# Performance work log

Hardware: AMD Instinct MI355X
Metric: run time of the kernel (lower is better)

The kernel has to match this reference:

```python
import jax, jax.numpy as jnp
import numpy as np

I3 = jnp.eye(3, dtype=jnp.float32)
G_VEC = jnp.array([0.0, 0.0, -9.80665], dtype=jnp.float32)
# Q diag: [cov_omega x3, cov_acc x3, cov_b_omega x3, cov_b_acc x3, cov_Rot_c_i x3, cov_t_c_i x3]
Q_DIAG = jnp.array([1e-3] * 3 + [1e-2] * 3 + [6e-9] * 3 + [2e-4] * 3 + [1e-9] * 3 + [1e-9] * 3, dtype=jnp.float32)
N_NORM_ROT = 100
N_NORM_ROT_CI = 1000


def skew(v):
    z = jnp.zeros_like(v[0])
    return jnp.stack([jnp.stack([z, -v[2], v[1]]),
                      jnp.stack([v[2], z, -v[0]]),
                      jnp.stack([-v[1], v[0], z])])


def so3exp(phi):
    a2 = jnp.sum(phi * phi)
    small = a2 < 1e-12
    a = jnp.sqrt(jnp.where(small, 1.0, a2))
    axis = phi / a
    c, s = jnp.cos(a), jnp.sin(a)
    big = c * I3 + (1.0 - c) * jnp.outer(axis, axis) + s * skew(axis)
    return jnp.where(small, I3 + skew(phi), big)


def sen3exp(xi):
    # SE_2(3) exponential: xi[:3]=rotation, xi[3:9]=(v, p) parts
    phi = xi[:3]
    a2 = jnp.sum(phi * phi)
    small = a2 < 1e-12
    a = jnp.sqrt(jnp.where(small, 1.0, a2))
    axis = phi / a
    c, s = jnp.cos(a), jnp.sin(a)
    sk = skew(axis)
    R = jnp.where(small, I3 + skew(phi),
                  c * I3 + (1.0 - c) * jnp.outer(axis, axis) + s * sk)
    J = jnp.where(small, I3 + 0.5 * skew(phi),
                  (s / a) * I3 + (1.0 - s / a) * jnp.outer(axis, axis) + ((1.0 - c) / a) * sk)
    x = J @ xi[3:].reshape(2, 3).T  # (3,2): columns are dv, dp
    return R, x


def normalize_rot(R):
    # Polar-factor re-orthonormalization (equivalent to the SVD-based
    # normalize_rot for near-rotation matrices), via Newton-Schulz iteration
    # which is smooth and jit/vjp friendly.
    def body(X, _):
        return 1.5 * X - 0.5 * (X @ X.T @ X), None
    X, _ = jax.lax.scan(body, R, None, length=8)
    return X


def from_rpy(roll, pitch, yaw):
    cr, sr = jnp.cos(roll), jnp.sin(roll)
    cp, sp = jnp.cos(pitch), jnp.sin(pitch)
    cy, sy = jnp.cos(yaw), jnp.sin(yaw)
    one = jnp.ones_like(cr)
    zero = jnp.zeros_like(cr)
    Rx = jnp.stack([jnp.stack([one, zero, zero]), jnp.stack([zero, cr, -sr]), jnp.stack([zero, sr, cr])])
    Ry = jnp.stack([jnp.stack([cp, zero, sp]), jnp.stack([zero, one, zero]), jnp.stack([-sp, zero, cp])])
    Rz = jnp.stack([jnp.stack([cy, -sy, zero]), jnp.stack([sy, cy, zero]), jnp.stack([zero, zero, one])])
    return Rz @ Ry @ Rx


def init_covariance():
    P = jnp.zeros((21, 21), dtype=jnp.float32)
    P = P.at[:2, :2].set(1e-3 * jnp.eye(2))     # cov_Rot0 (no yaw error)
    P = P.at[3:5, 3:5].set(0.1 * jnp.eye(2))    # cov_v0
    P = P.at[9:12, 9:12].set(6e-3 * I3)         # cov_b_omega0
    P = P.at[12:15, 12:15].set(4e-3 * I3)       # cov_b_acc0
    P = P.at[15:18, 15:18].set(1e-6 * I3)       # cov_Rot_c_i0
    P = P.at[18:21, 18:21].set(5e-3 * I3)       # cov_t_c_i0
    return P


def propagate_cov(P, Rot, v, p, dt):
    F = jnp.zeros((21, 21), dtype=P.dtype)
    F = F.at[3:6, :3].set(skew(G_VEC))
    F = F.at[6:9, 3:6].set(I3)
    F = F.at[:3, 9:12].set(-Rot)
    F = F.at[3:6, 9:12].set(-skew(v) @ Rot)
    F = F.at[3:6, 12:15].set(-Rot)
    F = F.at[6:9, 9:12].set(-skew(p) @ Rot)
    G = jnp.zeros((21, 18), dtype=P.dtype)
    G = G.at[:3, :3].set(Rot)
    G = G.at[3:6, 3:6].set(Rot)
    G = G.at[9:12, 6:9].set(I3)
    G = G.at[12:15, 9:12].set(I3)
    G = G.at[15:18, 12:15].set(I3)
    G = G.at[18:21, 15:18].set(I3)
    F = F * dt
    G = G * dt
    F2 = F @ F
    Phi = jnp.eye(21, dtype=P.dtype) + F + 0.5 * F2 + (F2 @ F) / 6.0  # 3rd-order expm
    return Phi @ (P + (G * Q_DIAG[None, :]) @ G.T) @ Phi.T


def _step(carry, xs):
    Rot, v, p, b_om, b_ac, Rci, tci, P = carry
    u_i, dt_i, mcov_i, i = xs
    # ---- propagate ----
    acc = Rot @ (u_i[3:6] - b_ac) + G_VEC
    v_n = v + acc * dt_i
    p_n = p + v * dt_i + 0.5 * acc * dt_i * dt_i
    Rot_n = Rot @ so3exp((u_i[:3] - b_om) * dt_i)
    P_n = propagate_cov(P, Rot, v, p, dt_i)
    # ---- update: zero lateral/vertical body-velocity pseudo-measurement ----
    omega = u_i[:3] - b_om
    Rot_body = Rot_n @ Rci
    v_imu = Rot_n.T @ v_n
    v_body = Rci.T @ v_imu + skew(tci) @ omega
    H = jnp.zeros((2, 21), dtype=P.dtype)
    H = H.at[:, 3:6].set(Rot_body.T[1:])
    H = H.at[:, 15:18].set((Rci.T @ skew(v_imu))[1:])
    H = H.at[:, 9:12].set(skew(tci)[1:])
    H = H.at[:, 18:21].set(-skew(omega)[1:])
    r = -v_body[1:]
    Rm = jnp.diag(mcov_i)
    S = H @ P_n @ H.T + Rm                    # (2,2)
    K = jnp.linalg.solve(S, H @ P_n).T        # K = P H^T S^-1 (P, S symmetric)
    dx = K @ r                                 # (21,)
    dR, dxi = sen3exp(dx[:9])
    Rot_u = dR @ Rot_n
    v_u = dR @ v_n + dxi[:, 0]
    p_u = dR @ p_n + dxi[:, 1]
    b_om_u = b_om + dx[9:12]
    b_ac_u = b_ac + dx[12:15]
    Rci_u = so3exp(dx[15:18]) @ Rci
    tci_u = tci + dx[18:21]
    IKH = jnp.eye(21, dtype=P.dtype) - K @ H
    P_u = IKH @ P_n @ IKH.T + K @ Rm @ K.T    # Joseph form
    P_u = 0.5 * (P_u + P_u.T)
    Rot_u = jnp.where(i % N_NORM_ROT == 0, normalize_rot(Rot_u), Rot_u)
    Rci_u = jnp.where(i % N_NORM_ROT_CI == 0, normalize_rot(Rci_u), Rci_u)
    carry = (Rot_u, v_u, p_u, b_om_u, b_ac_u, Rci_u, tci_u, P_u)
    return carry, (Rot_u, v_u, p_u, b_om_u, b_ac_u, Rci_u, tci_u)


def _forward(t, u, measurements_covs, v_mes, p_mes, ang0, N):
    dt = t[1:N] - t[:N - 1]
    Rot0 = from_rpy(ang0[0], ang0[1], ang0[2])
    z3 = jnp.zeros(3, dtype=u.dtype)
    carry0 = (Rot0, v_mes[0], z3, z3, z3, I3, z3, init_covariance())
    xs = (u[1:N], dt, measurements_covs[1:N], jnp.arange(1, N))
    _, ys = jax.lax.scan(_step, carry0, xs)
    Rot = jnp.concatenate([Rot0[None], ys[0]], axis=0)
    v = jnp.concatenate([v_mes[0][None], ys[1]], axis=0)
    p = jnp.concatenate([z3[None], ys[2]], axis=0)
    b_omega = jnp.concatenate([z3[None], ys[3]], axis=0)
    b_acc = jnp.concatenate([z3[None], ys[4]], axis=0)
    Rot_c_i = jnp.concatenate([I3[None], ys[5]], axis=0)
    t_c_i = jnp.concatenate([z3[None], ys[6]], axis=0)
    return (Rot, v, p, b_omega, b_acc, Rot_c_i, t_c_i)


def setup_inputs() -> dict:
    key = jax.random.key(0)
    N = 20000  # 200 s at 100 Hz IMU
    k0, k1, k2, k3, k4, k5 = jax.random.split(key, 6)
    t = jnp.arange(N, dtype=jnp.float32) * 0.01
    gyro = 0.01 * jax.random.normal(k0, (N, 3), dtype=jnp.float32)
    acc = jnp.array([0.0, 0.0, 9.80665], jnp.float32) + 0.1 * jax.random.normal(k1, (N, 3), dtype=jnp.float32)
    u = jnp.concatenate([gyro, acc], axis=1)
    measurements_covs = 0.1 + jax.random.uniform(k2, (N, 2), dtype=jnp.float32)
    v_mes = jax.random.normal(k3, (N, 3), dtype=jnp.float32)
    p_mes = jax.random.normal(k4, (N, 3), dtype=jnp.float32)
    ang0 = 0.01 * jax.random.normal(k5, (3,), dtype=jnp.float32)
    return dict(t=t, u=u, measurements_covs=measurements_covs, v_mes=v_mes, p_mes=p_mes, ang0=ang0, N=N)


def reference(t, u, measurements_covs, v_mes, p_mes, ang0, N):
    return _forward(t, u, measurements_covs, v_mes, p_mes, ang0, N)
```

## Files before the change

### kernel.cpp

```cpp
#include <hip/hip_runtime.h>

#define GRAV 9.80665f
#define WAVE_SYNC() do { \
    asm volatile("s_waitcnt lgkmcnt(0)" ::: "memory"); \
    __builtin_amdgcn_sched_barrier(0); \
  } while(0)

__device__ __forceinline__ float sel3(int r, float a0, float a1, float a2){
  float x = (r==1)? a1 : a0;
  return (r>=2)? a2 : x;
}
__device__ __forceinline__ float RL(float v, int k){
  return __int_as_float(__builtin_amdgcn_readlane(__float_as_int(v), k));
}
__device__ __forceinline__ float pick9(int k, const float* X){
  float s=X[0];
  s=(k==1)?X[1]:s; s=(k==2)?X[2]:s; s=(k==3)?X[3]:s; s=(k==4)?X[4]:s;
  s=(k==5)?X[5]:s; s=(k==6)?X[6]:s; s=(k==7)?X[7]:s; s=(k==8)?X[8]:s;
  return s;
}

__device__ __forceinline__ void mm33(float* __restrict__ O, const float* A, const float* B){
#pragma unroll
  for(int r=0;r<3;++r){
#pragma unroll
    for(int c=0;c<3;++c){
      O[r*3+c] = A[r*3+0]*B[0*3+c] + A[r*3+1]*B[1*3+c] + A[r*3+2]*B[2*3+c];
    }
  }
}

__device__ __forceinline__ void rot_from_t2(float t_, float p0, float p1, float p2, float* R){
  float c_, k1_, k2_;
  if (t_ < 1e-4f){
    c_  = 1.f - t_*(0.5f - t_*((1.f/24.f) - t_*(1.f/720.f)));
    k2_ = 1.f - t_*((1.f/6.f) - t_*((1.f/120.f) - t_*(1.f/5040.f)));
    k1_ = 0.5f - t_*((1.f/24.f) - t_*(1.f/720.f));
  } else {
    float a = sqrtf(t_);
    c_ = __cosf(a);
    float s = __sinf(a);
    k2_ = s/a;
    k1_ = (1.f - c_)/t_;
  }
  R[0]=c_+k1_*p0*p0;      R[1]=k1_*p0*p1-k2_*p2;  R[2]=k1_*p0*p2+k2_*p1;
  R[3]=k1_*p0*p1+k2_*p2;  R[4]=c_+k1_*p1*p1;      R[5]=k1_*p1*p2-k2_*p0;
  R[6]=k1_*p0*p2-k2_*p1;  R[7]=k1_*p1*p2+k2_*p0;  R[8]=c_+k1_*p2*p2;
}

__device__ __forceinline__ void normalize_rot9(float* X){
#pragma unroll 1
  for(int it=0; it<8; ++it){
    float Y[9], Z[9];
#pragma unroll
    for(int r=0;r<3;++r)
#pragma unroll
      for(int c=0;c<3;++c)
        Y[r*3+c] = X[r*3+0]*X[c*3+0] + X[r*3+1]*X[c*3+1] + X[r*3+2]*X[c*3+2];
#pragma unroll
    for(int r=0;r<3;++r)
#pragma unroll
      for(int c=0;c<3;++c)
        Z[r*3+c] = Y[r*3+0]*X[0*3+c] + Y[r*3+1]*X[1*3+c] + Y[r*3+2]*X[2*3+c];
#pragma unroll
    for(int e=0;e<9;++e) X[e] = 1.5f*X[e] - 0.5f*Z[e];
  }
}

__device__ __forceinline__ float pick_state(int l,
    const float* Rt, const float* vv, const float* pp,
    const float* bw, const float* ba, const float* Rc, const float* tc){
  float s = Rt[0];
  s=(l==1)?Rt[1]:s;  s=(l==2)?Rt[2]:s;  s=(l==3)?Rt[3]:s;  s=(l==4)?Rt[4]:s;
  s=(l==5)?Rt[5]:s;  s=(l==6)?Rt[6]:s;  s=(l==7)?Rt[7]:s;  s=(l==8)?Rt[8]:s;
  s=(l==9)?vv[0]:s;  s=(l==10)?vv[1]:s; s=(l==11)?vv[2]:s;
  s=(l==12)?pp[0]:s; s=(l==13)?pp[1]:s; s=(l==14)?pp[2]:s;
  s=(l==15)?bw[0]:s; s=(l==16)?bw[1]:s; s=(l==17)?bw[2]:s;
  s=(l==18)?ba[0]:s; s=(l==19)?ba[1]:s; s=(l==20)?ba[2]:s;
  s=(l==21)?Rc[0]:s; s=(l==22)?Rc[1]:s; s=(l==23)?Rc[2]:s;
  s=(l==24)?Rc[3]:s; s=(l==25)?Rc[4]:s; s=(l==26)?Rc[5]:s;
  s=(l==27)?Rc[6]:s; s=(l==28)?Rc[7]:s; s=(l==29)?Rc[8]:s;
  s=(l==30)?tc[0]:s; s=(l==31)?tc[1]:s; s=(l==32)?tc[2]:s;
  return s;
}

__global__ __launch_bounds__(64,1)
void iekf_scan_kernel(const float* __restrict__ t,
                      const float* __restrict__ u,
                      const float* __restrict__ mcov,
                      const float* __restrict__ v_mes,
                      const float* __restrict__ ang0,
                      float* __restrict__ out, int N)
{
  const int l = threadIdx.x;
  __shared__ float  Pm[441];
  __shared__ float  Eb[441];
  __shared__ float  PnS[441];
  __shared__ float2 HPs2[21];
  __shared__ __align__(16) float stS[36];

  for (int e=l; e<441; e+=64){
    int r=e/21, c=e-(e/21)*21;
    float vI=0.f;
    if (r==c){
      if (r<2) vI=0.001f;
      else if (r==3||r==4) vI=0.1f;
      else if (r>=9&&r<12) vI=0.006f;
      else if (r>=12&&r<15) vI=0.004f;
      else if (r>=15&&r<18) vI=1e-6f;
      else if (r>=18) vI=0.005f;
    }
    Pm[e]=vI;
  }

  int ostr=0; float* op = out;
  {
    int obase=0, ooff=0;
    if (l<9)       {obase=0;    ostr=9; ooff=l;}
    else if (l<12) {obase=9*N;  ostr=3; ooff=l-9;}
    else if (l<15) {obase=12*N; ostr=3; ooff=l-12;}
    else if (l<18) {obase=15*N; ostr=3; ooff=l-15;}
    else if (l<21) {obase=18*N; ostr=3; ooff=l-18;}
    else if (l<30) {obase=21*N; ostr=9; ooff=l-21;}
    else           {obase=30*N; ostr=3; ooff=l-30;}
    op = out + obase + ooff;
  }

  const int g21 = l/21;
  const int c21 = l - g21*21;
  const int cw  = 9 + 4*g21;
  int l1 = l+21; if (l1>=63) l1-=63;
  int l2 = l+42; if (l2>=63) l2-=63;
  static const int cols[12] = {3,4,5, 9,10,11, 15,16,17, 18,19,20};

  {
    float Rt0[9], vv0[3], pp0[3], bwa[3], baa[3], Rc0[9], tca[3];
    float rl = ang0[0], pt = ang0[1], yw = ang0[2];
    float cr=cosf(rl), sr=sinf(rl), cp=cosf(pt), sp=sinf(pt), cy=cosf(yw), sy=sinf(yw);
    Rt0[0]=cy*cp; Rt0[1]=cy*sp*sr - sy*cr; Rt0[2]=cy*sp*cr + sy*sr;
    Rt0[3]=sy*cp; Rt0[4]=sy*sp*sr + cy*cr; Rt0[5]=sy*sp*cr - cy*sr;
    Rt0[6]=-sp;   Rt0[7]=cp*sr;            Rt0[8]=cp*cr;
    vv0[0]=v_mes[0]; vv0[1]=v_mes[1]; vv0[2]=v_mes[2];
#pragma unroll
    for(int k=0;k<3;++k){ pp0[k]=0.f; bwa[k]=0.f; baa[k]=0.f; tca[k]=0.f; }
    Rc0[0]=1.f;Rc0[1]=0.f;Rc0[2]=0.f;Rc0[3]=0.f;Rc0[4]=1.f;Rc0[5]=0.f;Rc0[6]=0.f;Rc0[7]=0.f;Rc0[8]=1.f;
    float sv = pick_state(l, Rt0, vv0, pp0, bwa, baa, Rc0, tca);
    if (l<33){ op[0] = sv; stS[l] = sv; }
    if (l>=33 && l<36) stS[l] = 0.f;
  }
  WAVE_SYNC();

  float tA = t[0], tB = t[1];
  float cu[6];
#pragma unroll
  for(int k=0;k<6;++k) cu[k]=u[6+k];
  float cm0=mcov[2], cm1=mcov[3];

  int nx100=100, nx1000=1000;

#pragma unroll 1
  for (int i=1; i<N; ++i){
    float dt = tB - tA;
    float u0=cu[0], u1=cu[1], u2=cu[2], u3=cu[3], u4=cu[4], u5=cu[5];
    float crm0=cm0, crm1=cm1;
    if (i+1 < N){
      tA = tB; tB = t[i+1];
#pragma unroll
      for(int k=0;k<6;++k) cu[k]=u[(i+1)*6+k];
      cm0 = mcov[(i+1)*2]; cm1 = mcov[(i+1)*2+1];
    }

    const float4* st4 = (const float4*)stS;
    float4 q0=st4[0], q1=st4[1], q2=st4[2], q3=st4[3], q4=st4[4], q5=st4[5], q6=st4[6], q7=st4[7], q8=st4[8];
    float Rt[9] = {q0.x,q0.y,q0.z,q0.w,q1.x,q1.y,q1.z,q1.w,q2.x};
    float vv0s=q2.y, vv1s=q2.z, vv2s=q2.w;
    float pp0s=q3.x, pp1s=q3.y, pp2s=q3.z;
    float bw0=q3.w, bw1=q4.x, bw2=q4.y;
    float ba0=q4.z, ba1=q4.w, ba2=q5.x;
    float Rc[9] = {q5.y,q5.z,q5.w,q6.x,q6.y,q6.z,q6.w,q7.x,q7.y};
    float tc0=q7.z, tc1=q7.w, tc2=q8.x;

    float dt2=dt*dt, gdt=GRAV*dt, hdt=0.5f*dt, hdt2=0.5f*dt*dt;
    float hgdt2 = 0.5f*gdt*dt;
    float g6d   = gdt*dt2*(1.0f/6.0f);

    float w0=u0-bw0, w1=u1-bw1, w2=u2-bw2;
    float aa0=u3-ba0, aa1=u4-ba1, aa2=u5-ba2;
    float acc0 = Rt[0]*aa0+Rt[1]*aa1+Rt[2]*aa2;
    float acc1 = Rt[3]*aa0+Rt[4]*aa1+Rt[5]*aa2;
    float acc2 = Rt[6]*aa0+Rt[7]*aa1+Rt[8]*aa2 - GRAV;
    float vn0=vv0s+acc0*dt, vn1=vv1s+acc1*dt, vn2=vv2s+acc2*dt;
    float pn0=pp0s+vv0s*dt+acc0*hdt2;
    float pn1=pp1s+vv1s*dt+acc1*hdt2;
    float pn2=pp2s+vv2s*dt+acc2*hdt2;
    float ph0=w0*dt, ph1=w1*dt, ph2=w2*dt;
    float dRs[9]; rot_from_t2(ph0*ph0+ph1*ph1+ph2*ph2, ph0,ph1,ph2, dRs);
    float Rn[9]; mm33(Rn, Rt, dRs);

    float RtG[3], RtA[3], RtB[3];
#pragma unroll
    for(int k=0;k<3;++k){
      float r0=Rt[k], r3=Rt[3+k], r6=Rt[6+k];
      RtG[k] = sel3(g21, r0, r3, r6);
      RtA[k] = sel3(g21, r3, r6, r0);
      RtB[k] = sel3(g21, r6, r0, r3);
    }
    float vAs = sel3(g21, vv2s, vv0s, vv1s), vBs = sel3(g21, vv1s, vv2s, vv0s);
    float pAs = sel3(g21, pp2s, pp0s, pp1s), pBs = sel3(g21, pp1s, pp2s, pp0s);
    float Bs0,Bs1,Bs2, Cs0,Cs1,Cs2, Ds0,Ds1,Ds2;
    {
      float bs[3], cs[3], ds[3];
#pragma unroll
      for(int k=0;k<3;++k){
        bs[k] = -dt*RtG[k];
        float craw = dt*(vAs*RtA[k] - vBs*RtB[k]);
        float selC = sel3(g21, -RtA[k], RtB[k], 0.f);
        cs[k] = craw + hgdt2*selC;
        float draw = dt*(pAs*RtA[k] - pBs*RtB[k]);
        ds[k] = draw + hdt*craw + g6d*selC;
      }
      Bs0=bs[0];Bs1=bs[1];Bs2=bs[2];
      Cs0=cs[0];Cs1=cs[1];Cs2=cs[2];
      Ds0=ds[0];Ds1=ds[1];Ds2=ds[2];
    }

    float q0d=0.001f*dt2, q1d=0.01f*dt2;
    float q69=6e-9f*dt2, q24=2e-4f*dt2, q19=1e-9f*dt2;

    if (l<63){
      int c = c21;
      bool cl3 = (c<3);
      bool c36 = (c>=3 && c<6);
      int csel = c36 ? (c-3) : (cl3 ? c : 0);
      float Rtc0 = sel3(csel, Rt[0], Rt[3], Rt[6]);
      float Rtc1 = sel3(csel, Rt[1], Rt[4], Rt[7]);
      float Rtc2 = sel3(csel, Rt[2], Rt[5], Rt[8]);
      float dot0 = Rt[0]*Rtc0 + Rt[1]*Rtc1 + Rt[2]*Rtc2;
      float dot1 = Rt[3]*Rtc0 + Rt[4]*Rtc1 + Rt[5]*Rtc2;
      float dotg = RtG[0]*Rtc0 + RtG[1]*Rtc1 + RtG[2]*Rtc2;
      float d0  = cl3 ? q0d*dot0 : 0.f;
      float d1  = cl3 ? q0d*dot1 : 0.f;
      float dg  = cl3 ? q0d*dotg : 0.f;
      float dg3 = c36 ? q1d*dotg : 0.f;

      float m0  = Pm[c]            + d0;
      float m1  = Pm[21+c]         + d1;
      float mr  = Pm[g21*21+c]     + dg;
      float m3r = Pm[(3+g21)*21+c] + dg3;
      float m6r = Pm[(6+g21)*21+c];
      float m9  = Pm[9*21+c]  + ((c==9) ? q69 : 0.f);
      float m10 = Pm[10*21+c] + ((c==10)? q69 : 0.f);
      float m11 = Pm[11*21+c] + ((c==11)? q69 : 0.f);
      float m12 = Pm[12*21+c] + ((c==12)? q24 : 0.f);
      float m13 = Pm[13*21+c] + ((c==13)? q24 : 0.f);
      float m14 = Pm[14*21+c] + ((c==14)? q24 : 0.f);

      float Ar = (g21==0)? gdt*m1 : (g21==1)? -gdt*m0 : 0.f;
      float bterm = Bs0*m12+Bs1*m13+Bs2*m14;
      float e0 = mr + Bs0*m9+Bs1*m10+Bs2*m11;
      float e1 = m3r + Ar + Cs0*m9+Cs1*m10+Cs2*m11 + bterm;
      float e2 = m6r + hdt*Ar + dt*m3r + Ds0*m9+Ds1*m10+Ds2*m11 + hdt*bterm;
      Eb[g21*21+c]=e0; Eb[(3+g21)*21+c]=e1; Eb[(6+g21)*21+c]=e2;
#pragma unroll
      for (int jj=0;jj<4;++jj){
        int row = cw+jj;
        float qd = (row<12)? q69 : (row<15)? q24 : q19;
        Eb[row*21+c] = Pm[row*21+c] + ((row==c)? qd : 0.f);
      }
    }

    float H0[12], H1[12];
    float vi0, vi1, vi2, rr0, rr1;
    {
      float Rb1 = Rn[0]*Rc[1]+Rn[1]*Rc[4]+Rn[2]*Rc[7];
      float Rb4 = Rn[3]*Rc[1]+Rn[4]*Rc[4]+Rn[5]*Rc[7];
      float Rb7 = Rn[6]*Rc[1]+Rn[7]*Rc[4]+Rn[8]*Rc[7];
      float Rb2 = Rn[0]*Rc[2]+Rn[1]*Rc[5]+Rn[2]*Rc[8];
      float Rb5 = Rn[3]*Rc[2]+Rn[4]*Rc[5]+Rn[5]*Rc[8];
      float Rb8 = Rn[6]*Rc[2]+Rn[7]*Rc[5]+Rn[8]*Rc[8];
      vi0 = Rn[0]*vn0+Rn[3]*vn1+Rn[6]*vn2;
      vi1 = Rn[1]*vn0+Rn[4]*vn1+Rn[7]*vn2;
      vi2 = Rn[2]*vn0+Rn[5]*vn1+Rn[8]*vn2;
      float vb1 = Rc[1]*vi0+Rc[4]*vi1+Rc[7]*vi2 + (tc2*w0 - tc0*w2);
      float vb2 = Rc[2]*vi0+Rc[5]*vi1+Rc[8]*vi2 + (tc0*w1 - tc1*w0);
      rr0 = -vb1; rr1 = -vb2;
      H0[0]=Rb1; H0[1]=Rb4; H0[2]=Rb7;
      H1[0]=Rb2; H1[1]=Rb5; H1[2]=Rb8;
      H0[3]=tc2;  H0[4]=0.f;  H0[5]=-tc0;
      H1[3]=-tc1; H1[4]=tc0;  H1[5]=0.f;
      H0[6]=Rc[4]*vi2 - Rc[7]*vi1;  H0[7]=Rc[7]*vi0 - Rc[1]*vi2;  H0[8]=Rc[1]*vi1 - Rc[4]*vi0;
      H1[6]=Rc[5]*vi2 - Rc[8]*vi1;  H1[7]=Rc[8]*vi0 - Rc[2]*vi2;  H1[8]=Rc[2]*vi1 - Rc[5]*vi0;
      H0[9]=-w2; H0[10]=0.f; H0[11]=w0;
      H1[9]=w1;  H1[10]=-w0; H1[11]=0.f;
    }
    WAVE_SYNC();

    float pnv[7];
#pragma unroll
    for(int k=0;k<7;++k) pnv[k]=0.f;
    float p0=0.f, p1=0.f;
    if (l<63){
      int r = c21;
      const float* Er = Eb + r*21;
      float e0a=Er[0], e1a=Er[1];
      float eg=Er[g21], e3g=Er[3+g21], e6g=Er[6+g21];
      float e9=Er[9],e10=Er[10],e11=Er[11],e12=Er[12],e13=Er[13],e14=Er[14];
      float Ag = (g21==0)? gdt*e1a : (g21==1)? -gdt*e0a : 0.f;
      float bterm = Bs0*e12+Bs1*e13+Bs2*e14;
      pnv[0] = eg + Bs0*e9+Bs1*e10+Bs2*e11;
      pnv[1] = e3g + Ag + Cs0*e9+Cs1*e10+Cs2*e11 + bterm;
      pnv[2] = e6g + hdt*Ag + dt*e3g + Ds0*e9+Ds1*e10+Ds2*e11 + hdt*bterm;
      pnv[3] = Er[cw]; pnv[4] = Er[cw+1]; pnv[5] = Er[cw+2]; pnv[6] = Er[cw+3];

      PnS[r*21 + g21]   = pnv[0];
      PnS[r*21 + 3+g21] = pnv[1];
      PnS[r*21 + 6+g21] = pnv[2];
      PnS[r*21 + cw]    = pnv[3];
      PnS[r*21 + cw+1]  = pnv[4];
      PnS[r*21 + cw+2]  = pnv[5];
      PnS[r*21 + cw+3]  = pnv[6];

      float c1a = sel3(g21, H0[0], H0[1], H0[2]);
      float c3a = sel3(g21, H0[3], 0.f,   H0[8]);
      float c4a = sel3(g21, H0[4], 0.f,   H0[9]);
      float c5a = sel3(g21, H0[5], H0[6], H0[10]);
      float c6a = sel3(g21, 0.f,   H0[7], H0[11]);
      float c1b = sel3(g21, H1[0], H1[1], H1[2]);
      float c3b = sel3(g21, H1[3], 0.f,   H1[8]);
      float c4b = sel3(g21, H1[4], 0.f,   H1[9]);
      float c5b = sel3(g21, H1[5], H1[6], H1[10]);
      float c6b = sel3(g21, 0.f,   H1[7], H1[11]);
      p0 = c1a*pnv[1] + c3a*pnv[3] + c4a*pnv[4] + c5a*pnv[5] + c6a*pnv[6];
      p1 = c1b*pnv[1] + c3b*pnv[3] + c4b*pnv[4] + c5b*pnv[5] + c6b*pnv[6];
    }
    float hpr0 = p0 + __shfl(p0, l1) + __shfl(p0, l2);
    float hpr1 = p1 + __shfl(p1, l1) + __shfl(p1, l2);
    if (l<21) HPs2[l] = make_float2(hpr0, hpr1);

    float hph00=0.f, hph01=0.f, hph10=0.f, hph11=0.f;
#pragma unroll
    for(int k=0;k<12;++k){
      float hp0 = RL(hpr0, cols[k]);
      float hp1 = RL(hpr1, cols[k]);
      hph00 += hp0*H0[k]; hph01 += hp0*H1[k];
      hph10 += hp1*H0[k]; hph11 += hp1*H1[k];
    }
    float s00 = hph00 + crm0, s01 = hph01, s10 = hph10, s11 = hph11 + crm1;
    float idet = 1.0f/(s00*s11 - s01*s10);
    float i00 =  s11*idet, i01 = -s01*idet, i10 = -s10*idet, i11 = s00*idet;
    float K0 = i00*hpr0 + i01*hpr1;
    float K1 = i10*hpr0 + i11*hpr1;
    float s01q = 0.5f*(s01 + s10);
    float dxval = K0*rr0 + K1*rr1;

    float dx0 = RL(dxval,0), dx1 = RL(dxval,1), dx2 = RL(dxval,2);
    float dx3 = RL(dxval,3), dx4 = RL(dxval,4), dx5 = RL(dxval,5);
    float dx6 = RL(dxval,6), dx7 = RL(dxval,7), dx8 = RL(dxval,8);
    float dx15 = RL(dxval,15), dx16 = RL(dxval,16), dx17 = RL(dxval,17);
    int src = (l>=30 && l<33)? (l-12) : ((l>=15 && l<21)? (l-6) : 0);
    float dxadd = __shfl(dxval, src);

    float t2x = dx0*dx0+dx1*dx1+dx2*dx2;
    float cX,k1X,k2X,j1X;
    if (t2x < 1e-4f){
      cX  = 1.f - t2x*(0.5f - t2x*((1.f/24.f) - t2x*(1.f/720.f)));
      k2X = 1.f - t2x*((1.f/6.f) - t2x*((1.f/120.f) - t2x*(1.f/5040.f)));
      k1X = 0.5f - t2x*((1.f/24.f) - t2x*(1.f/720.f));
      j1X = (1.f/6.f) - t2x*((1.f/120.f) - t2x*(1.f/5040.f));
    } else {
      float a = sqrtf(t2x);
      cX = __cosf(a);
      float s = __sinf(a);
      k2X = s/a; k1X = (1.f-cX)/t2x; j1X = (1.f-k2X)/t2x;
    }
    float dR[9];
    dR[0]=cX+k1X*dx0*dx0;      dR[1]=k1X*dx0*dx1-k2X*dx2; dR[2]=k1X*dx0*dx2+k2X*dx1;
    dR[3]=k1X*dx0*dx1+k2X*dx2; dR[4]=cX+k1X*dx1*dx1;      dR[5]=k1X*dx1*dx2-k2X*dx0;
    dR[6]=k1X*dx0*dx2-k2X*dx1; dR[7]=k1X*dx1*dx2+k2X*dx0; dR[8]=cX+k1X*dx2*dx2;
    float Jm[9];
    Jm[0]=k2X+j1X*dx0*dx0;      Jm[1]=j1X*dx0*dx1-k1X*dx2; Jm[2]=j1X*dx0*dx2+k1X*dx1;
    Jm[3]=j1X*dx0*dx1+k1X*dx2;  Jm[4]=k2X+j1X*dx1*dx1;     Jm[5]=j1X*dx1*dx2-k1X*dx0;
    Jm[6]=j1X*dx0*dx2-k1X*dx1;  Jm[7]=j1X*dx1*dx2+k1X*dx0; Jm[8]=k2X+j1X*dx2*dx2;
    float Ec[9];
    rot_from_t2(dx15*dx15+dx16*dx16+dx17*dx17, dx15,dx16,dx17, Ec);

    WAVE_SYNC();

    if (l<63){
      int r = c21;
#pragma unroll
      for (int s=0;s<7;++s){
        int j = (s<3)? (g21 + 3*s) : (cw + (s-3));
        float pnT = PnS[j*21 + r];
        float2 hpj = HPs2[j];
        float kjx = i00*hpj.x + i01*hpj.y;
        float kjy = i10*hpj.x + i11*hpj.y;
        float base  = 0.5f*(pnv[s] + pnT);
        float cross = (K0*hpj.x + K1*hpj.y) + (kjx*hpr0 + kjy*hpr1);
        float quad  = (K0*kjx)*s00 + (K0*kjy + K1*kjx)*s01q + (K1*kjy)*s11;
        Pm[r*21+j] = base - cross + quad;
      }
    }

    float myval = 0.f;
    if (l<9){
      int ro=(l>=6)?2:((l>=3)?1:0); int co=l-3*ro;
      float d0=sel3(ro,dR[0],dR[3],dR[6]), d1=sel3(ro,dR[1],dR[4],dR[7]), d2=sel3(ro,dR[2],dR[5],dR[8]);
      float n0=sel3(co,Rn[0],Rn[1],Rn[2]), n1=sel3(co,Rn[3],Rn[4],Rn[5]), n2=sel3(co,Rn[6],Rn[7],Rn[8]);
      myval = d0*n0 + d1*n1 + d2*n2;
    } else if (l<15){
      int j=l-9; bool isv=(j<3); int ro = isv? j : (j-3);
      float x0 = isv? vn0:pn0, x1 = isv? vn1:pn1, x2 = isv? vn2:pn2;
      float y0 = isv? dx3:dx6, y1 = isv? dx4:dx7, y2 = isv? dx5:dx8;
      float d0=sel3(ro,dR[0],dR[3],dR[6]), d1=sel3(ro,dR[1],dR[4],dR[7]), d2=sel3(ro,dR[2],dR[5],dR[8]);
      float j0=sel3(ro,Jm[0],Jm[3],Jm[6]), j1m=sel3(ro,Jm[1],Jm[4],Jm[7]), j2m=sel3(ro,Jm[2],Jm[5],Jm[8]);
      myval = d0*x0 + d1*x1 + d2*x2 + j0*y0 + j1m*y1 + j2m*y2;
    } else if (l<21){
      float old = (l<18)? sel3(l-15,bw0,bw1,bw2) : sel3(l-18,ba0,ba1,ba2);
      myval = old + dxadd;
    } else if (l<30){
      int j=l-21; int ro=(j>=6)?2:((j>=3)?1:0); int co=j-3*ro;
      float e0=sel3(ro,Ec[0],Ec[3],Ec[6]), e1=sel3(ro,Ec[1],Ec[4],Ec[7]), e2=sel3(ro,Ec[2],Ec[5],Ec[8]);
      float r0=sel3(co,Rc[0],Rc[1],Rc[2]), r1=sel3(co,Rc[3],Rc[4],Rc[5]), r2=sel3(co,Rc[6],Rc[7],Rc[8]);
      myval = e0*r0 + e1*r1 + e2*r2;
    } else if (l<33){
      myval = sel3(l-30,tc0,tc1,tc2) + dxadd;
    }
    if (l<33) stS[l] = myval;

    bool n100 = (i==nx100), n1000 = (i==nx1000);
    if (n100) nx100 += 100;
    if (n1000) nx1000 += 1000;
    if (n100 || n1000){
      WAVE_SYNC();
      if (n100){
        float X[9];
#pragma unroll
        for (int k=0;k<9;++k) X[k]=stS[k];
        normalize_rot9(X);
        if (l<9){ myval = pick9(l,X); stS[l] = myval; }
      }
      if (n1000){
        float Y[9];
#pragma unroll
        for (int k=0;k<9;++k) Y[k]=stS[21+k];
        normalize_rot9(Y);
        if (l>=21 && l<30){ myval = pick9(l-21,Y); stS[l] = myval; }
      }
    }

    if (l<33) op[i*ostr] = myval;

    WAVE_SYNC();
  }
}

extern "C" void kernel_launch(void* const* d_in, const int* in_sizes, int n_in,
                              void* d_out, int out_size, void* d_ws, size_t ws_size,
                              hipStream_t stream) {
  (void)n_in; (void)out_size; (void)d_ws; (void)ws_size;
  const float* t     = (const float*)d_in[0];
  const float* u     = (const float*)d_in[1];
  const float* mcov  = (const float*)d_in[2];
  const float* v_mes = (const float*)d_in[3];
  const float* ang0  = (const float*)d_in[5];
  int N = in_sizes[0];
  iekf_scan_kernel<<<dim3(1), dim3(64), 0, stream>>>(t, u, mcov, v_mes, ang0, (float*)d_out, N);
}
```

Baseline: 44.76 ms.

## Keep filter state in registers and pad covariance rows for vector LDS loads

```diff
diff --git a/kernel.cpp b/kernel.cpp
--- a/kernel.cpp
+++ b/kernel.cpp
@@ -5,6 +5,8 @@
     asm volatile("s_waitcnt lgkmcnt(0)" ::: "memory"); \
     __builtin_amdgcn_sched_barrier(0); \
   } while(0)
+
+#define LDP 28
 
 __device__ __forceinline__ float sel3(int r, float a0, float a1, float a2){
   float x = (r==1)? a1 : a0;
@@ -93,14 +95,11 @@
                       float* __restrict__ out, int N)
 {
   const int l = threadIdx.x;
-  __shared__ float  Pm[441];
-  __shared__ float  Eb[441];
-  __shared__ float  PnS[441];
-  __shared__ float2 HPs2[21];
-  __shared__ __align__(16) float stS[36];
-
-  for (int e=l; e<441; e+=64){
-    int r=e/21, c=e-(e/21)*21;
+  __shared__ __align__(16) float Pm[21*LDP];
+  __shared__ __align__(16) float Eb[21*LDP];
+
+  for (int e=l; e<21*LDP; e+=64){
+    int r=e/LDP, c=e-(e/LDP)*LDP;
     float vI=0.f;
     if (r==c){
       if (r<2) vI=0.001f;
@@ -108,7 +107,7 @@
       else if (r>=9&&r<12) vI=0.006f;
       else if (r>=12&&r<15) vI=0.004f;
       else if (r>=15&&r<18) vI=1e-6f;
-      else if (r>=18) vI=0.005f;
+      else if (r>=18&&r<21) vI=0.005f;
     }
     Pm[e]=vI;
   }
@@ -133,6 +132,7 @@
   int l2 = l+42; if (l2>=63) l2-=63;
   static const int cols[12] = {3,4,5, 9,10,11, 15,16,17, 18,19,20};
 
+  float myval = 0.f;
   {
     float Rt0[9], vv0[3], pp0[3], bwa[3], baa[3], Rc0[9], tca[3];
     float rl = ang0[0], pt = ang0[1], yw = ang0[2];
@@ -145,8 +145,7 @@
     for(int k=0;k<3;++k){ pp0[k]=0.f; bwa[k]=0.f; baa[k]=0.f; tca[k]=0.f; }
     Rc0[0]=1.f;Rc0[1]=0.f;Rc0[2]=0.f;Rc0[3]=0.f;Rc0[4]=1.f;Rc0[5]=0.f;Rc0[6]=0.f;Rc0[7]=0.f;Rc0[8]=1.f;
     float sv = pick_state(l, Rt0, vv0, pp0, bwa, baa, Rc0, tca);
-    if (l<33){ op[0] = sv; stS[l] = sv; }
-    if (l>=33 && l<36) stS[l] = 0.f;
+    if (l<33){ op[0] = sv; myval = sv; }
   }
   WAVE_SYNC();
 
@@ -170,15 +169,17 @@
       cm0 = mcov[(i+1)*2]; cm1 = mcov[(i+1)*2+1];
     }
 
-    const float4* st4 = (const float4*)stS;
-    float4 q0=st4[0], q1=st4[1], q2=st4[2], q3=st4[3], q4=st4[4], q5=st4[5], q6=st4[6], q7=st4[7], q8=st4[8];
-    float Rt[9] = {q0.x,q0.y,q0.z,q0.w,q1.x,q1.y,q1.z,q1.w,q2.x};
-    float vv0s=q2.y, vv1s=q2.z, vv2s=q2.w;
-    float pp0s=q3.x, pp1s=q3.y, pp2s=q3.z;
-    float bw0=q3.w, bw1=q4.x, bw2=q4.y;
-    float ba0=q4.z, ba1=q4.w, ba2=q5.x;
-    float Rc[9] = {q5.y,q5.z,q5.w,q6.x,q6.y,q6.z,q6.w,q7.x,q7.y};
-    float tc0=q7.z, tc1=q7.w, tc2=q8.x;
+    float Rt[9];
+#pragma unroll
+    for(int k=0;k<9;++k) Rt[k] = RL(myval, k);
+    float vv0s=RL(myval,9),  vv1s=RL(myval,10), vv2s=RL(myval,11);
+    float pp0s=RL(myval,12), pp1s=RL(myval,13), pp2s=RL(myval,14);
+    float bw0=RL(myval,15),  bw1=RL(myval,16),  bw2=RL(myval,17);
+    float ba0=RL(myval,18),  ba1=RL(myval,19),  ba2=RL(myval,20);
+    float Rc[9];
+#pragma unroll
+    for(int k=0;k<9;++k) Rc[k] = RL(myval, 21+k);
+    float tc0=RL(myval,30), tc1=RL(myval,31), tc2=RL(myval,32);
 
     float dt2=dt*dt, gdt=GRAV*dt, hdt=0.5f*dt, hdt2=0.5f*dt*dt;
     float hgdt2 = 0.5f*gdt*dt;
@@ -229,6 +230,10 @@
 
     if (l<63){
       int c = c21;
+      const float4* Pr4 = (const float4*)(Pm + c*LDP);
+      float4 a0=Pr4[0], a1=Pr4[1], a2=Pr4[2], a3=Pr4[3], a4=Pr4[4];
+      float m20 = Pm[c*LDP + 20];
+
       bool cl3 = (c<3);
       bool c36 = (c>=3 && c<6);
       int csel = c36 ? (c-3) : (cl3 ? c : 0);
@@ -238,39 +243,42 @@
       float dot0 = Rt[0]*Rtc0 + Rt[1]*Rtc1 + Rt[2]*Rtc2;
       float dot1 = Rt[3]*Rtc0 + Rt[4]*Rtc1 + Rt[5]*Rtc2;
       float dotg = RtG[0]*Rtc0 + RtG[1]*Rtc1 + RtG[2]*Rtc2;
-      float d0  = cl3 ? q0d*dot0 : 0.f;
-      float d1  = cl3 ? q0d*dot1 : 0.f;
-      float dg  = cl3 ? q0d*dotg : 0.f;
-      float dg3 = c36 ? q1d*dotg : 0.f;
-
-      float m0  = Pm[c]            + d0;
-      float m1  = Pm[21+c]         + d1;
-      float mr  = Pm[g21*21+c]     + dg;
-      float m3r = Pm[(3+g21)*21+c] + dg3;
-      float m6r = Pm[(6+g21)*21+c];
-      float m9  = Pm[9*21+c]  + ((c==9) ? q69 : 0.f);
-      float m10 = Pm[10*21+c] + ((c==10)? q69 : 0.f);
-      float m11 = Pm[11*21+c] + ((c==11)? q69 : 0.f);
-      float m12 = Pm[12*21+c] + ((c==12)? q24 : 0.f);
-      float m13 = Pm[13*21+c] + ((c==13)? q24 : 0.f);
-      float m14 = Pm[14*21+c] + ((c==14)? q24 : 0.f);
+
+      float m0  = a0.x + (cl3 ? q0d*dot0 : 0.f);
+      float m1  = a0.y + (cl3 ? q0d*dot1 : 0.f);
+      float mr  = sel3(g21, a0.x, a0.y, a0.z) + (cl3 ? q0d*dotg : 0.f);
+      float m3r = sel3(g21, a0.w, a1.x, a1.y) + (c36 ? q1d*dotg : 0.f);
+      float m6r = sel3(g21, a1.z, a1.w, a2.x);
+      float m9  = a2.y + ((c==9) ? q69 : 0.f);
+      float m10 = a2.z + ((c==10)? q69 : 0.f);
+      float m11 = a2.w + ((c==11)? q69 : 0.f);
+      float m12 = a3.x + ((c==12)? q24 : 0.f);
+      float m13 = a3.y + ((c==13)? q24 : 0.f);
+      float m14 = a3.z + ((c==14)? q24 : 0.f);
 
       float Ar = (g21==0)? gdt*m1 : (g21==1)? -gdt*m0 : 0.f;
       float bterm = Bs0*m12+Bs1*m13+Bs2*m14;
       float e0 = mr + Bs0*m9+Bs1*m10+Bs2*m11;
       float e1 = m3r + Ar + Cs0*m9+Cs1*m10+Cs2*m11 + bterm;
       float e2 = m6r + hdt*Ar + dt*m3r + Ds0*m9+Ds1*m10+Ds2*m11 + hdt*bterm;
-      Eb[g21*21+c]=e0; Eb[(3+g21)*21+c]=e1; Eb[(6+g21)*21+c]=e2;
-#pragma unroll
-      for (int jj=0;jj<4;++jj){
-        int row = cw+jj;
-        float qd = (row<12)? q69 : (row<15)? q24 : q19;
-        Eb[row*21+c] = Pm[row*21+c] + ((row==c)? qd : 0.f);
-      }
+      Eb[g21*LDP+c]=e0; Eb[(3+g21)*LDP+c]=e1; Eb[(6+g21)*LDP+c]=e2;
+
+      float mc0 = sel3(g21, a2.y, a3.y, a4.y);
+      float mc1 = sel3(g21, a2.z, a3.z, a4.z);
+      float mc2 = sel3(g21, a2.w, a3.w, a4.w);
+      float mc3 = sel3(g21, a3.x, a4.x, m20);
+      float qd0 = sel3(g21, q69, q24, q19);
+      float qd1 = sel3(g21, q69, q24, q19);
+      float qd2 = sel3(g21, q69, q19, q19);
+      float qd3 = sel3(g21, q24, q19, q19);
+      Eb[(cw+0)*LDP+c] = mc0 + ((cw+0==c)? qd0 : 0.f);
+      Eb[(cw+1)*LDP+c] = mc1 + ((cw+1==c)? qd1 : 0.f);
+      Eb[(cw+2)*LDP+c] = mc2 + ((cw+2==c)? qd2 : 0.f);
+      Eb[(cw+3)*LDP+c] = mc3 + ((cw+3==c)? qd3 : 0.f);
     }
 
     float H0[12], H1[12];
-    float vi0, vi1, vi2, rr0, rr1;
+    float rr0, rr1;
     {
       float Rb1 = Rn[0]*Rc[1]+Rn[1]*Rc[4]+Rn[2]*Rc[7];
       float Rb4 = Rn[3]*Rc[1]+Rn[4]*Rc[4]+Rn[5]*Rc[7];
@@ -278,9 +286,9 @@
       float Rb2 = Rn[0]*Rc[2]+Rn[1]*Rc[5]+Rn[2]*Rc[8];
       float Rb5 = Rn[3]*Rc[2]+Rn[4]*Rc[5]+Rn[5]*Rc[8];
       float Rb8 = Rn[6]*Rc[2]+Rn[7]*Rc[5]+Rn[8]*Rc[8];
-      vi0 = Rn[0]*vn0+Rn[3]*vn1+Rn[6]*vn2;
-      vi1 = Rn[1]*vn0+Rn[4]*vn1+Rn[7]*vn2;
-      vi2 = Rn[2]*vn0+Rn[5]*vn1+Rn[8]*vn2;
+      float vi0 = Rn[0]*vn0+Rn[3]*vn1+Rn[6]*vn2;
+      float vi1 = Rn[1]*vn0+Rn[4]*vn1+Rn[7]*vn2;
+      float vi2 = Rn[2]*vn0+Rn[5]*vn1+Rn[8]*vn2;
       float vb1 = Rc[1]*vi0+Rc[4]*vi1+Rc[7]*vi2 + (tc2*w0 - tc0*w2);
       float vb2 = Rc[2]*vi0+Rc[5]*vi1+Rc[8]*vi2 + (tc0*w1 - tc1*w0);
       rr0 = -vb1; rr1 = -vb2;
@@ -301,24 +309,25 @@
     float p0=0.f, p1=0.f;
     if (l<63){
       int r = c21;
-      const float* Er = Eb + r*21;
-      float e0a=Er[0], e1a=Er[1];
-      float eg=Er[g21], e3g=Er[3+g21], e6g=Er[6+g21];
-      float e9=Er[9],e10=Er[10],e11=Er[11],e12=Er[12],e13=Er[13],e14=Er[14];
+      const float4* Er4 = (const float4*)(Eb + r*LDP);
+      float4 a0=Er4[0], a1=Er4[1], a2=Er4[2], a3=Er4[3], a4=Er4[4];
+      float e20 = Eb[r*LDP + 20];
+
+      float e0a=a0.x, e1a=a0.y;
+      float eg  = sel3(g21, a0.x, a0.y, a0.z);
+      float e3g = sel3(g21, a0.w, a1.x, a1.y);
+      float e6g = sel3(g21, a1.z, a1.w, a2.x);
+      float e9=a2.y, e10=a2.z, e11=a2.w, e12=a3.x, e13=a3.y, e14=a3.z;
+
       float Ag = (g21==0)? gdt*e1a : (g21==1)? -gdt*e0a : 0.f;
       float bterm = Bs0*e12+Bs1*e13+Bs2*e14;
       pnv[0] = eg + Bs0*e9+Bs1*e10+Bs2*e11;
       pnv[1] = e3g + Ag + Cs0*e9+Cs1*e10+Cs2*e11 + bterm;
       pnv[2] = e6g + hdt*Ag + dt*e3g + Ds0*e9+Ds1*e10+Ds2*e11 + hdt*bterm;
-      pnv[3] = Er[cw]; pnv[4] = Er[cw+1]; pnv[5] = Er[cw+2]; pnv[6] = Er[cw+3];
-
-      PnS[r*21 + g21]   = pnv[0];
-      PnS[r*21 + 3+g21] = pnv[1];
-      PnS[r*21 + 6+g21] = pnv[2];
-      PnS[r*21 + cw]    = pnv[3];
-      PnS[r*21 + cw+1]  = pnv[4];
-      PnS[r*21 + cw+2]  = pnv[5];
-      PnS[r*21 + cw+3]  = pnv[6];
+      pnv[3] = sel3(g21, a2.y, a3.y, a4.y);
+      pnv[4] = sel3(g21, a2.z, a3.z, a4.z);
+      pnv[5] = sel3(g21, a2.w, a3.w, a4.w);
+      pnv[6] = sel3(g21, a3.x, a4.x, e20);
 
       float c1a = sel3(g21, H0[0], H0[1], H0[2]);
       float c3a = sel3(g21, H0[3], 0.f,   H0[8]);
@@ -335,7 +344,14 @@
     }
     float hpr0 = p0 + __shfl(p0, l1) + __shfl(p0, l2);
     float hpr1 = p1 + __shfl(p1, l1) + __shfl(p1, l2);
-    if (l<21) HPs2[l] = make_float2(hpr0, hpr1);
+
+    float hpjx[7], hpjy[7];
+#pragma unroll
+    for (int s=0;s<7;++s){
+      int j = (s<3)? (g21 + 3*s) : (cw + (s-3));
+      hpjx[s] = __shfl(hpr0, j);
+      hpjy[s] = __shfl(hpr1, j);
+    }
 
     float hph00=0.f, hph01=0.f, hph10=0.f, hph11=0.f;
 #pragma unroll
@@ -359,6 +375,23 @@
     float dx15 = RL(dxval,15), dx16 = RL(dxval,16), dx17 = RL(dxval,17);
     int src = (l>=30 && l<33)? (l-12) : ((l>=15 && l<21)? (l-6) : 0);
     float dxadd = __shfl(dxval, src);
+
+    if (l<63){
+      int r = c21;
+#pragma unroll
+      for (int s=0;s<7;++s){
+        int j = (s<3)? (g21 + 3*s) : (cw + (s-3));
+        float kjx = i00*hpjx[s] + i01*hpjy[s];
+        float kjy = i10*hpjx[s] + i11*hpjy[s];
+        float cross = (K0*hpjx[s] + K1*hpjy[s]) + (kjx*hpr0 + kjy*hpr1);
+        float quad  = (K0*kjx)*s00 + (K0*kjy + K1*kjx)*s01q + (K1*kjy)*s11;
+        float val = pnv[s] - cross + quad;
+        if (r <= j){
+          Pm[r*LDP+j] = val;
+          if (r < j) Pm[j*LDP+r] = val;
+        }
+      }
+    }
 
     float t2x = dx0*dx0+dx1*dx1+dx2*dx2;
     float cX,k1X,k2X,j1X;
@@ -384,68 +417,49 @@
     float Ec[9];
     rot_from_t2(dx15*dx15+dx16*dx16+dx17*dx17, dx15,dx16,dx17, Ec);
 
-    WAVE_SYNC();
-
-    if (l<63){
-      int r = c21;
-#pragma unroll
-      for (int s=0;s<7;++s){
-        int j = (s<3)? (g21 + 3*s) : (cw + (s-3));
-        float pnT = PnS[j*21 + r];
-        float2 hpj = HPs2[j];
-        float kjx = i00*hpj.x + i01*hpj.y;
-        float kjy = i10*hpj.x + i11*hpj.y;
-        float base  = 0.5f*(pnv[s] + pnT);
-        float cross = (K0*hpj.x + K1*hpj.y) + (kjx*hpr0 + kjy*hpr1);
-        float quad  = (K0*kjx)*s00 + (K0*kjy + K1*kjx)*s01q + (K1*kjy)*s11;
-        Pm[r*21+j] = base - cross + quad;
-      }
-    }
-
-    float myval = 0.f;
+    float nv = 0.f;
     if (l<9){
       int ro=(l>=6)?2:((l>=3)?1:0); int co=l-3*ro;
       float d0=sel3(ro,dR[0],dR[3],dR[6]), d1=sel3(ro,dR[1],dR[4],dR[7]), d2=sel3(ro,dR[2],dR[5],dR[8]);
       float n0=sel3(co,Rn[0],Rn[1],Rn[2]), n1=sel3(co,Rn[3],Rn[4],Rn[5]), n2=sel3(co,Rn[6],Rn[7],Rn[8]);
-      myval = d0*n0 + d1*n1 + d2*n2;
+      nv = d0*n0 + d1*n1 + d2*n2;
     } else if (l<15){
       int j=l-9; bool isv=(j<3); int ro = isv? j : (j-3);
       float x0 = isv? vn0:pn0, x1 = isv? vn1:pn1, x2 = isv? vn2:pn2;
       float y0 = isv? dx3:dx6, y1 = isv? dx4:dx7, y2 = isv? dx5:dx8;
       float d0=sel3(ro,dR[0],dR[3],dR[6]), d1=sel3(ro,dR[1],dR[4],dR[7]), d2=sel3(ro,dR[2],dR[5],dR[8]);
       float j0=sel3(ro,Jm[0],Jm[3],Jm[6]), j1m=sel3(ro,Jm[1],Jm[4],Jm[7]), j2m=sel3(ro,Jm[2],Jm[5],Jm[8]);
-      myval = d0*x0 + d1*x1 + d2*x2 + j0*y0 + j1m*y1 + j2m*y2;
+      nv = d0*x0 + d1*x1 + d2*x2 + j0*y0 + j1m*y1 + j2m*y2;
     } else if (l<21){
       float old = (l<18)? sel3(l-15,bw0,bw1,bw2) : sel3(l-18,ba0,ba1,ba2);
-      myval = old + dxadd;
+      nv = old + dxadd;
     } else if (l<30){
       int j=l-21; int ro=(j>=6)?2:((j>=3)?1:0); int co=j-3*ro;
       float e0=sel3(ro,Ec[0],Ec[3],Ec[6]), e1=sel3(ro,Ec[1],Ec[4],Ec[7]), e2=sel3(ro,Ec[2],Ec[5],Ec[8]);
       float r0=sel3(co,Rc[0],Rc[1],Rc[2]), r1=sel3(co,Rc[3],Rc[4],Rc[5]), r2=sel3(co,Rc[6],Rc[7],Rc[8]);
-      myval = e0*r0 + e1*r1 + e2*r2;
+      nv = e0*r0 + e1*r1 + e2*r2;
     } else if (l<33){
-      myval = sel3(l-30,tc0,tc1,tc2) + dxadd;
-    }
-    if (l<33) stS[l] = myval;
+      nv = sel3(l-30,tc0,tc1,tc2) + dxadd;
+    }
+    if (l<33) myval = nv;
 
     bool n100 = (i==nx100), n1000 = (i==nx1000);
     if (n100) nx100 += 100;
     if (n1000) nx1000 += 1000;
     if (n100 || n1000){
-      WAVE_SYNC();
       if (n100){
         float X[9];
 #pragma unroll
-        for (int k=0;k<9;++k) X[k]=stS[k];
+        for (int k=0;k<9;++k) X[k]=RL(myval,k);
         normalize_rot9(X);
-        if (l<9){ myval = pick9(l,X); stS[l] = myval; }
+        if (l<9) myval = pick9(l,X);
       }
       if (n1000){
         float Y[9];
 #pragma unroll
-        for (int k=0;k<9;++k) Y[k]=stS[21+k];
+        for (int k=0;k<9;++k) Y[k]=RL(myval,21+k);
         normalize_rot9(Y);
-        if (l>=21 && l<30){ myval = pick9(l-21,Y); stS[l] = myval; }
+        if (l>=21 && l<30) myval = pick9(l-21,Y);
       }
     }
 
```

New measurement: 49.86 ms. +11.4%, slower.
